# Kernel tuning notes

Hardware: AMD Instinct MI355X
Metric: run time of the kernel (lower is better)

Reference implementation:

```python
import jax, jax.numpy as jnp
import numpy as np


def setup_inputs() -> dict:
    key = jax.random.key(0)
    k1, k2, k3 = jax.random.split(key, 3)
    in_features, out_features = 256, 256
    x = jax.random.normal(k1, (16, 128, in_features), dtype=jnp.float32)
    # weight[:, :, 0] = output mixing weights, weight[:, :, 1] = frequency weights
    weight = jax.random.normal(k2, (in_features, out_features, 2), dtype=jnp.float32) / np.sqrt(in_features)
    # bias[0] = output bias, bias[1:] = per-(in,out) phase
    bias = jax.random.normal(k3, (in_features + 1, out_features), dtype=jnp.float32) / np.sqrt(in_features)
    return {"x": x, "weight": weight, "bias": bias}


def reference(x, weight, bias):
    out_features = weight.shape[1]
    out_shape = x.shape[:-1] + (out_features,)
    xf = x.reshape(-1, x.shape[-1])  # [B, I]
    w_amp = weight[:, :, 0]   # [I, O]
    w_freq = weight[:, :, 1]  # [I, O]
    # bio = sin(x_bi * w_io + phase_io); out_bo = sum_i amp_io * bio
    bio = jnp.sin(jnp.einsum('bi,io->bio', xf, w_freq) + bias[1:, :])
    out = jnp.einsum('io,bio->bo', w_amp, bio) + bias[0, :]
    return out.reshape(out_shape)
```

## Files before the change

### kernel.cpp

```cpp
#include <hip/hip_runtime.h>


typedef _Float16 f16;
typedef _Float16 f16x8 __attribute__((ext_vector_type(8)));
typedef float f32x4 __attribute__((ext_vector_type(4)));

constexpr int IN_F  = 256;
constexpr int OUT_F = 256;
constexpr int BROWS = 2048;
constexpr int NJ    = 9;
constexpr int KTOT  = NJ * IN_F;
constexpr int BM = 32, BN = 32, BK = 64;
constexpr int NSTEP = KTOT / BK;
constexpr int XPAD  = 260;
#define XS 0.25f
#define INV2PI 0.15915494309189535f

__global__ __launch_bounds__(256) void prep_B(const float* __restrict__ w,
                                              const float* __restrict__ bias,
                                              f16* __restrict__ BT,
                                              float* __restrict__ bias2) {
    const int o = blockIdx.x;
    const int i = threadIdx.x;
    const float amp = w[(i * OUT_F + o) * 2 + 0];
    const float fr  = w[(i * OUT_F + o) * 2 + 1];
    const float p   = bias[(1 + i) * OUT_F + o];
    const float sp = __builtin_amdgcn_sinf(p * INV2PI);
    const float cp = __builtin_amdgcn_cosf(p * INV2PI);
    const float f4 = 4.0f * fr;

    float s = amp * sp;
#pragma unroll
    for (int off = 32; off > 0; off >>= 1) s += __shfl_down(s, off);
    __shared__ float rbuf[4];
    if ((i & 63) == 0) rbuf[i >> 6] = s;
    __syncthreads();
    if (i == 0) bias2[o] = bias[o] + rbuf[0] + rbuf[1] + rbuf[2] + rbuf[3];

    const float SC[10] = {
        1.0f,            1.0f,
       -0.5f,           -1.666666667e-1f,
        4.166666667e-2f, 8.333333333e-3f,
       -1.388888889e-3f,-1.984126984e-4f,
        2.480158730e-5f, 2.755731922e-6f
    };
    float pw = f4;
#pragma unroll
    for (int j = 1; j <= NJ; ++j) {
        const float trig = (j & 1) ? cp : sp;
        BT[(size_t)o * KTOT + (j - 1) * IN_F + i] = (f16)(amp * trig * SC[j] * pw);
        pw *= f4;
    }
}

__global__ __launch_bounds__(256) void gemm(const float* __restrict__ x,
                                            const f16* __restrict__ BT,
                                            const float* __restrict__ bias2,
                                            float* __restrict__ out) {
    __shared__ __align__(16) float xp[BM][XPAD];
    __shared__ __align__(16) f16 Bs[2][BN][BK + 8];

    const int d  = blockIdx.x;
    const int n0 = (d & 7) * BN;
    const int m0 = (d >> 3) * BM;

    const int t = threadIdx.x;
    const int l = t & 63;
    const int w = t >> 6;
    const int wm = (w >> 1) * 16;
    const int wn = (w & 1) * 16;
    const int fra = l & 15;
    const int fk  = (l >> 4) * 8;

    const int ro = t & 31;
    const int c0 = (t >> 5) * 32;
    float xq[32], xpr[32];
#pragma unroll
    for (int q = 0; q < 8; ++q) {
        const f32x4 v = *(const f32x4*)(x + (size_t)(m0 + ro) * IN_F + c0 + q * 4);
#pragma unroll
        for (int e = 0; e < 4; ++e) { xq[q * 4 + e] = v[e] * XS; xpr[q * 4 + e] = v[e] * XS; }
    }
#pragma unroll
    for (int q = 0; q < 8; ++q) {
        f32x4 v = { xpr[q * 4], xpr[q * 4 + 1], xpr[q * 4 + 2], xpr[q * 4 + 3] };
        *(f32x4*)&xp[ro][c0 + q * 4] = v;
    }

    const int br = t >> 3;
    const int bc = (t & 7) * 8;
    const f16* bt_base = BT + (size_t)(n0 + br) * KTOT + bc;
    uint4 bv = *(const uint4*)(bt_base);
    *(uint4*)&Bs[0][br][bc] = bv;
    bv = *(const uint4*)(bt_base + BK);
    __syncthreads();

    f32x4 acc = {0.f, 0.f, 0.f, 0.f};

    for (int ts = 0; ts < NSTEP; ++ts) {
        const int i0 = (ts & 3) * BK;
#pragma unroll
        for (int h = 0; h < 2; ++h) {
            const f32x4 a0 = *(const f32x4*)&xp[wm + fra][i0 + h * 32 + fk];
            const f32x4 a1 = *(const f32x4*)&xp[wm + fra][i0 + h * 32 + fk + 4];
            const f16x8 af = { (f16)a0[0], (f16)a0[1], (f16)a0[2], (f16)a0[3],
                               (f16)a1[0], (f16)a1[1], (f16)a1[2], (f16)a1[3] };
            const f16x8 bf = *(const f16x8*)&Bs[ts & 1][wn + fra][h * 32 + fk];
            acc = __builtin_amdgcn_mfma_f32_16x16x32_f16(af, bf, acc, 0, 0, 0);
        }
        if (ts + 1 < NSTEP) {
            *(uint4*)&Bs[(ts + 1) & 1][br][bc] = bv;
            if (ts + 2 < NSTEP) bv = *(const uint4*)(bt_base + (size_t)(ts + 2) * BK);
        }
        if ((ts & 3) == 3 && ts + 1 < NSTEP) {
            __syncthreads();
#pragma unroll
            for (int q = 0; q < 8; ++q) {
                f32x4 v;
#pragma unroll
                for (int e = 0; e < 4; ++e) { xpr[q * 4 + e] *= xq[q * 4 + e]; v[e] = xpr[q * 4 + e]; }
                *(f32x4*)&xp[ro][c0 + q * 4] = v;
            }
        }
        __syncthreads();
    }

    const int col = n0 + wn + (l & 15);
    const int r0  = (l >> 4) * 4;
    const float bb = bias2[col];
#pragma unroll
    for (int r = 0; r < 4; ++r) {
        out[(size_t)(m0 + wm + r0 + r) * OUT_F + col] = acc[r] + bb;
    }
}

extern "C" void kernel_launch(void* const* d_in, const int* in_sizes, int n_in,
                              void* d_out, int out_size, void* d_ws, size_t ws_size,
                              hipStream_t stream) {
    const float* x      = (const float*)d_in[0];
    const float* weight = (const float*)d_in[1];
    const float* bias   = (const float*)d_in[2];
    float* out          = (float*)d_out;

    f16* BT      = (f16*)d_ws;
    float* bias2 = (float*)((char*)d_ws + 1179648);

    prep_B<<<dim3(OUT_F), dim3(IN_F), 0, stream>>>(weight, bias, BT, bias2);
    gemm<<<dim3((BROWS / BM) * (OUT_F / BN)), dim3(256), 0, stream>>>(x, BT, bias2, out);
}
```

Measured before the change: 77.58 us.

## Fuse weight prep and GEMM into one cooperative persistent kernel

Merges the prep_B and gemm kernels into a single cooperative kernel that uses a grid-wide sync, removing one launch and the gap between the two kernels. The grid shrinks to 256 blocks, each computing two M tiles. B fragments are now read directly from global memory into registers with a one-step prefetch, replacing the shared-memory staging of B. x powers are stored in shared memory as fp16 instead of fp32. The costs are grid-sync overhead, half the parallelism of the old 512-block grid, and more register pressure from holding 16 B fragments per thread.

New measurement: 130.2 us. 1.68x slower.

```diff
diff --git a/kernel.cpp b/kernel.cpp
--- a/kernel.cpp
+++ b/kernel.cpp
@@ -1,5 +1,8 @@
 #include <hip/hip_runtime.h>
+#include <hip/hip_cooperative_groups.h>
 
+
+namespace cg = cooperative_groups;
 
 typedef _Float16 f16;
 typedef _Float16 f16x8 __attribute__((ext_vector_type(8)));
@@ -10,127 +13,130 @@
 constexpr int BROWS = 2048;
 constexpr int NJ    = 9;
 constexpr int KTOT  = NJ * IN_F;
-constexpr int BM = 32, BN = 32, BK = 64;
-constexpr int NSTEP = KTOT / BK;
-constexpr int XPAD  = 260;
+constexpr int BM = 32, BN = 32;
+constexpr int XPAD = 264;
 #define XS 0.25f
 #define INV2PI 0.15915494309189535f
 
-__global__ __launch_bounds__(256) void prep_B(const float* __restrict__ w,
-                                              const float* __restrict__ bias,
-                                              f16* __restrict__ BT,
-                                              float* __restrict__ bias2) {
-    const int o = blockIdx.x;
-    const int i = threadIdx.x;
-    const float amp = w[(i * OUT_F + o) * 2 + 0];
-    const float fr  = w[(i * OUT_F + o) * 2 + 1];
-    const float p   = bias[(1 + i) * OUT_F + o];
-    const float sp = __builtin_amdgcn_sinf(p * INV2PI);
-    const float cp = __builtin_amdgcn_cosf(p * INV2PI);
-    const float f4 = 4.0f * fr;
+__global__ __launch_bounds__(256, 2) void fused(
+    const float* __restrict__ x,
+    const float* __restrict__ w,
+    const float* __restrict__ bias,
+    f16* __restrict__ BT,
+    float* __restrict__ bias2,
+    float* __restrict__ out)
+{
+    __shared__ __align__(16) f16 xp16[BM][XPAD];
+    __shared__ float rbuf[4];
 
-    float s = amp * sp;
+    const int d = blockIdx.x;
+    const int t = threadIdx.x;
+
+    {
+        const int o = d, i = t;
+        const float amp = w[(i * OUT_F + o) * 2 + 0];
+        const float fr  = w[(i * OUT_F + o) * 2 + 1];
+        const float p   = bias[(1 + i) * OUT_F + o];
+        const float sp = __builtin_amdgcn_sinf(p * INV2PI);
+        const float cp = __builtin_amdgcn_cosf(p * INV2PI);
+        const float f4 = 4.0f * fr;
+
+        float s = amp * sp;
 #pragma unroll
-    for (int off = 32; off > 0; off >>= 1) s += __shfl_down(s, off);
-    __shared__ float rbuf[4];
-    if ((i & 63) == 0) rbuf[i >> 6] = s;
-    __syncthreads();
-    if (i == 0) bias2[o] = bias[o] + rbuf[0] + rbuf[1] + rbuf[2] + rbuf[3];
+        for (int off = 32; off > 0; off >>= 1) s += __shfl_down(s, off);
+        if ((i & 63) == 0) rbuf[i >> 6] = s;
+        __syncthreads();
+        if (i == 0) bias2[o] = bias[o] + rbuf[0] + rbuf[1] + rbuf[2] + rbuf[3];
 
-    const float SC[10] = {
-        1.0f,            1.0f,
-       -0.5f,           -1.666666667e-1f,
-        4.166666667e-2f, 8.333333333e-3f,
-       -1.388888889e-3f,-1.984126984e-4f,
-        2.480158730e-5f, 2.755731922e-6f
-    };
-    float pw = f4;
+        const float SC[10] = {
+            1.0f,            1.0f,
+           -0.5f,           -1.666666667e-1f,
+            4.166666667e-2f, 8.333333333e-3f,
+           -1.388888889e-3f,-1.984126984e-4f,
+            2.480158730e-5f, 2.755731922e-6f
+        };
+        float pw = f4;
 #pragma unroll
-    for (int j = 1; j <= NJ; ++j) {
-        const float trig = (j & 1) ? cp : sp;
-        BT[(size_t)o * KTOT + (j - 1) * IN_F + i] = (f16)(amp * trig * SC[j] * pw);
-        pw *= f4;
+        for (int j = 1; j <= NJ; ++j) {
+            BT[(size_t)o * KTOT + (j - 1) * IN_F + i] =
+                (f16)(amp * ((j & 1) ? cp : sp) * SC[j] * pw);
+            pw *= f4;
+        }
+        __threadfence();
     }
-}
 
-__global__ __launch_bounds__(256) void gemm(const float* __restrict__ x,
-                                            const f16* __restrict__ BT,
-                                            const float* __restrict__ bias2,
-                                            float* __restrict__ out) {
-    __shared__ __align__(16) float xp[BM][XPAD];
-    __shared__ __align__(16) f16 Bs[2][BN][BK + 8];
+    cg::this_grid().sync();
 
-    const int d  = blockIdx.x;
-    const int n0 = (d & 7) * BN;
-    const int m0 = (d >> 3) * BM;
-
-    const int t = threadIdx.x;
-    const int l = t & 63;
-    const int w = t >> 6;
-    const int wm = (w >> 1) * 16;
-    const int wn = (w & 1) * 16;
+    const int n0  = (d & 7) * BN;
+    const int l   = t & 63;
+    const int wv  = t >> 6;
+    const int wm  = (wv >> 1) * 16;
+    const int wn  = (wv & 1) * 16;
     const int fra = l & 15;
     const int fk  = (l >> 4) * 8;
+    const int ro  = t & 31;
+    const int c0  = (t >> 5) * 32;
 
-    const int ro = t & 31;
-    const int c0 = (t >> 5) * 32;
-    float xq[32], xpr[32];
-#pragma unroll
-    for (int q = 0; q < 8; ++q) {
-        const f32x4 v = *(const f32x4*)(x + (size_t)(m0 + ro) * IN_F + c0 + q * 4);
-#pragma unroll
-        for (int e = 0; e < 4; ++e) { xq[q * 4 + e] = v[e] * XS; xpr[q * 4 + e] = v[e] * XS; }
-    }
-#pragma unroll
-    for (int q = 0; q < 8; ++q) {
-        f32x4 v = { xpr[q * 4], xpr[q * 4 + 1], xpr[q * 4 + 2], xpr[q * 4 + 3] };
-        *(f32x4*)&xp[ro][c0 + q * 4] = v;
-    }
-
-    const int br = t >> 3;
-    const int bc = (t & 7) * 8;
-    const f16* bt_base = BT + (size_t)(n0 + br) * KTOT + bc;
-    uint4 bv = *(const uint4*)(bt_base);
-    *(uint4*)&Bs[0][br][bc] = bv;
-    bv = *(const uint4*)(bt_base + BK);
-    __syncthreads();
-
-    f32x4 acc = {0.f, 0.f, 0.f, 0.f};
-
-    for (int ts = 0; ts < NSTEP; ++ts) {
-        const int i0 = (ts & 3) * BK;
-#pragma unroll
-        for (int h = 0; h < 2; ++h) {
-            const f32x4 a0 = *(const f32x4*)&xp[wm + fra][i0 + h * 32 + fk];
-            const f32x4 a1 = *(const f32x4*)&xp[wm + fra][i0 + h * 32 + fk + 4];
-            const f16x8 af = { (f16)a0[0], (f16)a0[1], (f16)a0[2], (f16)a0[3],
-                               (f16)a1[0], (f16)a1[1], (f16)a1[2], (f16)a1[3] };
-            const f16x8 bf = *(const f16x8*)&Bs[ts & 1][wn + fra][h * 32 + fk];
-            acc = __builtin_amdgcn_mfma_f32_16x16x32_f16(af, bf, acc, 0, 0, 0);
-        }
-        if (ts + 1 < NSTEP) {
-            *(uint4*)&Bs[(ts + 1) & 1][br][bc] = bv;
-            if (ts + 2 < NSTEP) bv = *(const uint4*)(bt_base + (size_t)(ts + 2) * BK);
-        }
-        if ((ts & 3) == 3 && ts + 1 < NSTEP) {
-            __syncthreads();
-#pragma unroll
-            for (int q = 0; q < 8; ++q) {
-                f32x4 v;
-#pragma unroll
-                for (int e = 0; e < 4; ++e) { xpr[q * 4 + e] *= xq[q * 4 + e]; v[e] = xpr[q * 4 + e]; }
-                *(f32x4*)&xp[ro][c0 + q * 4] = v;
-            }
-        }
-        __syncthreads();
-    }
-
+    const f16* brow = BT + (size_t)(n0 + wn + fra) * KTOT + fk;
     const int col = n0 + wn + (l & 15);
     const int r0  = (l >> 4) * 4;
     const float bb = bias2[col];
+
+    for (int tt = 0; tt < 2; ++tt) {
+        const int m0 = ((d + tt * 256) >> 3) * BM;
+
+        float xq[32], xpr[32];
 #pragma unroll
-    for (int r = 0; r < 4; ++r) {
-        out[(size_t)(m0 + wm + r0 + r) * OUT_F + col] = acc[r] + bb;
+        for (int q = 0; q < 8; ++q) {
+            const f32x4 v = *(const f32x4*)(x + (size_t)(m0 + ro) * IN_F + c0 + q * 4);
+#pragma unroll
+            for (int e = 0; e < 4; ++e) { const float sv = v[e] * XS; xq[q * 4 + e] = sv; xpr[q * 4 + e] = sv; }
+        }
+        __syncthreads();
+#pragma unroll
+        for (int q = 0; q < 4; ++q) {
+            f16 h[8];
+#pragma unroll
+            for (int e = 0; e < 8; ++e) h[e] = (f16)xpr[q * 8 + e];
+            *(uint4*)&xp16[ro][c0 + q * 8] = *(const uint4*)h;
+        }
+        __syncthreads();
+
+        f32x4 acc = {0.f, 0.f, 0.f, 0.f};
+        f16x8 bnx[8];
+#pragma unroll
+        for (int u = 0; u < 8; ++u) bnx[u] = *(const f16x8*)(brow + u * 32);
+
+        for (int j = 1; j <= NJ; ++j) {
+            f16x8 bc[8];
+#pragma unroll
+            for (int u = 0; u < 8; ++u) bc[u] = bnx[u];
+            if (j < NJ) {
+#pragma unroll
+                for (int u = 0; u < 8; ++u)
+                    bnx[u] = *(const f16x8*)(brow + (size_t)j * IN_F + u * 32);
+            }
+            if (j > 1) {
+                __syncthreads();
+#pragma unroll
+                for (int q = 0; q < 4; ++q) {
+                    f16 h[8];
+#pragma unroll
+                    for (int e = 0; e < 8; ++e) { xpr[q * 8 + e] *= xq[q * 8 + e]; h[e] = (f16)xpr[q * 8 + e]; }
+                    *(uint4*)&xp16[ro][c0 + q * 8] = *(const uint4*)h;
+                }
+                __syncthreads();
+            }
+#pragma unroll
+            for (int u = 0; u < 8; ++u) {
+                const f16x8 af = *(const f16x8*)&xp16[wm + fra][u * 32 + fk];
+                acc = __builtin_amdgcn_mfma_f32_16x16x32_f16(af, bc[u], acc, 0, 0, 0);
+            }
+        }
+
+#pragma unroll
+        for (int r = 0; r < 4; ++r)
+            out[(size_t)(m0 + wm + r0 + r) * OUT_F + col] = acc[r] + bb;
     }
 }
 
@@ -145,6 +151,7 @@
     f16* BT      = (f16*)d_ws;
     float* bias2 = (float*)((char*)d_ws + 1179648);
 
-    prep_B<<<dim3(OUT_F), dim3(IN_F), 0, stream>>>(weight, bias, BT, bias2);
-    gemm<<<dim3((BROWS / BM) * (OUT_F / BN)), dim3(256), 0, stream>>>(x, BT, bias2, out);
+    void* args[] = { (void*)&x, (void*)&weight, (void*)&bias,
+                     (void*)&BT, (void*)&bias2, (void*)&out };
+    hipLaunchCooperativeKernel((void*)fused, dim3(256), dim3(256), args, 0, stream);
 }
```
